# Optimization experiments

Measured on AMD Instinct MI355X. Metric: run time of the kernel, lower is better.

## Reference

```python
import jax, jax.numpy as jnp
import numpy as np

EPS_DIR = 1e-15
EPS_W = 1e-5
NEAR_MIN = 0.05


def setup_inputs() -> dict:
    key = jax.random.key(0)
    k1, k2, k3 = jax.random.split(key, 3)
    B, N, T = 1, 262144, 128
    rays_o = jax.random.normal(k1, (B, N, 3), dtype=jnp.float32)
    rays_d = jax.random.normal(k2, (B, N, 3), dtype=jnp.float32)
    weights = jax.random.uniform(k3, (B * N, T - 1), dtype=jnp.float32)
    return {"rays_o": rays_o, "rays_d": rays_d, "weights": weights,
            "bound": 1, "n_samples": 128}


def _near_far_cube(ro, rd, bound):
    # ro, rd: [R, 3]
    tmin = (-bound - ro) / (rd + EPS_DIR)
    tmax = (bound - ro) / (rd + EPS_DIR)
    near = jnp.max(jnp.minimum(tmin, tmax), axis=-1, keepdims=True)  # [R,1]
    far = jnp.min(jnp.maximum(tmin, tmax), axis=-1, keepdims=True)   # [R,1]
    near = jnp.maximum(near, NEAR_MIN)
    return near, far


def _sample_pdf(bins, weights, n_samples):
    # bins: [R, T], weights: [R, T-1]; deterministic (det=True) inverse-CDF sampling
    w = weights + EPS_W
    pdf = w / jnp.sum(w, axis=-1, keepdims=True)
    cdf = jnp.cumsum(pdf, axis=-1)
    cdf = jnp.concatenate([jnp.zeros_like(cdf[..., :1]), cdf], axis=-1)  # [R, T]
    n = n_samples
    u = jnp.linspace(0.5 / n, 1.0 - 0.5 / n, n, dtype=cdf.dtype)
    u = jnp.broadcast_to(u, cdf.shape[:-1] + (n,))                        # [R, n]
    inds = jax.vmap(lambda c, uu: jnp.searchsorted(c, uu, side='right'))(cdf, u)
    T = cdf.shape[-1]
    below = jnp.maximum(inds - 1, 0)
    above = jnp.minimum(inds, T - 1)
    cdf_lo = jnp.take_along_axis(cdf, below, axis=-1)
    cdf_hi = jnp.take_along_axis(cdf, above, axis=-1)
    bin_lo = jnp.take_along_axis(bins, below, axis=-1)
    bin_hi = jnp.take_along_axis(bins, above, axis=-1)
    denom = cdf_hi - cdf_lo
    denom = jnp.where(denom < EPS_W, jnp.ones_like(denom), denom)
    t = (u - cdf_lo) / denom
    return bin_lo + t * (bin_hi - bin_lo)  # [R, n]


def reference(rays_o, rays_d, weights, bound, n_samples):
    ro = rays_o.reshape(-1, 3)
    rd = rays_d.reshape(-1, 3)
    near, far = _near_far_cube(ro, rd, float(bound))          # [R,1]
    T = weights.shape[-1] + 1
    z = jnp.linspace(0.0, 1.0, T, dtype=ro.dtype)[None, :]    # [1,T]
    z_vals = near + (far - near) * z                          # [R,T] coarse bins
    new_z_vals = _sample_pdf(z_vals, weights, n_samples)      # [R,n_samples]
    return new_z_vals
```

## Files before the change

kernel.cpp:

```cpp
#include <hip/hip_runtime.h>

#define EPS_DIR 1e-15f
#define EPS_W   1e-5f
#define NEAR_MIN 0.05f

__global__ __launch_bounds__(256) void nerf_sample_pdf_kernel(
    const float* __restrict__ rays_o,
    const float* __restrict__ rays_d,
    const float* __restrict__ weights,
    const int*   __restrict__ bound_p,
    float*       __restrict__ out,
    int R, int Tm1, int n)
{
    const int lane = threadIdx.x & 63;
    const int wid  = threadIdx.x >> 6;
    int ray = blockIdx.x * 4 + wid;
    const bool valid = (ray < R);
    if (!valid) ray = R - 1;

    __shared__ float cdf_s[4][132];
    float* __restrict__ cdf = cdf_s[wid];

    const float* __restrict__ wrow = weights + (size_t)ray * Tm1;
    const int i0 = 2 * lane, i1 = 2 * lane + 1;
    float w0 = (i0 < Tm1) ? (wrow[i0] + EPS_W) : 0.0f;
    float w1 = (i1 < Tm1) ? (wrow[i1] + EPS_W) : 0.0f;

    float S = w0 + w1;
#pragma unroll
    for (int off = 1; off < 64; off <<= 1) {
        float y = __shfl_up(S, off, 64);
        if (lane >= off) S += y;
    }
    const float total = __shfl(S, 63, 64);
    const float rinv  = __builtin_amdgcn_rcpf(total);
    float prevS = __shfl_up(S, 1, 64);
    if (lane == 0) prevS = 0.0f;

    cdf[i0] = prevS * rinv;
    cdf[i1] = (prevS + w0) * rinv;
    __syncthreads();

    const float b = (float)bound_p[0];
    float nearv = -3.4e38f, farv = 3.4e38f;
#pragma unroll
    for (int k = 0; k < 3; ++k) {
        float o = rays_o[(size_t)ray * 3 + k];
        float d = rays_d[(size_t)ray * 3 + k] + EPS_DIR;
        float r = __builtin_amdgcn_rcpf(d);
        float t0 = (-b - o) * r;
        float t1 = ( b - o) * r;
        nearv = fmaxf(nearv, fminf(t0, t1));
        farv  = fminf(farv,  fmaxf(t0, t1));
    }
    nearv = fmaxf(nearv, NEAR_MIN);
    const float scale = (farv - nearv) * __builtin_amdgcn_rcpf((float)Tm1);
    const float inv_n = 1.0f / (float)n;

    float* __restrict__ orow = out + (size_t)ray * n;

    for (int base = 0; base < n; base += 128) {
        const int j = base + 2 * lane;
        if (j >= n) break;
        const float u0 = ((float)j + 0.5f) * inv_n;
        const float u1 = u0 + inv_n;

        int   p0 = 0,   p1 = 0;
        float v0 = 0.f, v1 = 0.f;
#pragma unroll
        for (int step = 64; step >= 1; step >>= 1) {
            const float c0 = cdf[p0 + step];
            const float c1 = cdf[p1 + step];
            if (c0 <= u0) { p0 += step; v0 = c0; }
            if (c1 <= u1) { p1 += step; v1 = c1; }
        }
        const int a0 = (p0 < Tm1) ? p0 + 1 : Tm1;
        const int a1 = (p1 < Tm1) ? p1 + 1 : Tm1;
        const float h0 = cdf[a0];
        const float h1 = cdf[a1];
        const float d0 = h0 - v0;
        const float d1 = h1 - v1;
        const float t0 = (u0 - v0) * ((d0 < EPS_W) ? 1.0f : __builtin_amdgcn_rcpf(d0));
        const float t1 = (u1 - v1) * ((d1 < EPS_W) ? 1.0f : __builtin_amdgcn_rcpf(d1));
        const float z0 = fmaf(t0, (float)(a0 - p0) * scale, fmaf((float)p0, scale, nearv));
        const float z1 = fmaf(t1, (float)(a1 - p1) * scale, fmaf((float)p1, scale, nearv));

        if (valid) {
            if (j + 1 < n) {
                *reinterpret_cast<float2*>(orow + j) = make_float2(z0, z1);
            } else {
                orow[j] = z0;
            }
        }
    }
}

extern "C" void kernel_launch(void* const* d_in, const int* in_sizes, int n_in,
                              void* d_out, int out_size, void* d_ws, size_t ws_size,
                              hipStream_t stream) {
    const float* rays_o  = (const float*)d_in[0];
    const float* rays_d  = (const float*)d_in[1];
    const float* weights = (const float*)d_in[2];
    const int*   bound_p = (const int*)d_in[3];
    float*       out     = (float*)d_out;

    const int R   = in_sizes[0] / 3;
    const int Tm1 = in_sizes[2] / R;
    const int n   = out_size / R;

    dim3 grid((R + 3) / 4), block(256);
    nerf_sample_pdf_kernel<<<grid, block, 0, stream>>>(
        rays_o, rays_d, weights, bound_p, out, R, Tm1, n);
}
```

Before: 295.4 us.

## Add specialized kernel mapping eight threads per ray for T=128 shapes

Adds a kernel for the 127-weight, 128-sample shape in which 8 threads share one ray. Each thread loads 16 weights, computes a serial local prefix and combines across the 8 threads with an xor shuffle scan, then does 16 binary searches and writes float4 stores. This replaces a full 64-lane shuffle scan per ray and gives 32 rays per block, at the cost of more registers per thread and strided, uncoalesced weight loads. The generic kernel also gains bounds guards on its search, and the host picks the path based on shape.

```diff
diff --git a/kernel.cpp b/kernel.cpp
--- a/kernel.cpp
+++ b/kernel.cpp
@@ -4,7 +4,103 @@
 #define EPS_W   1e-5f
 #define NEAR_MIN 0.05f
 
-__global__ __launch_bounds__(256) void nerf_sample_pdf_kernel(
+__global__ __launch_bounds__(256) void nerf_sample_pdf_127_128(
+    const float* __restrict__ rays_o,
+    const float* __restrict__ rays_d,
+    const float* __restrict__ weights,
+    const int*   __restrict__ bound_p,
+    float*       __restrict__ out,
+    int R)
+{
+    const int t    = threadIdx.x;
+    const int g    = t & 7;
+    const int rloc = t >> 3;
+    int ray = blockIdx.x * 32 + rloc;
+    const bool valid = (ray < R);
+    if (!valid) ray = R - 1;
+
+    __shared__ float cdf_s[32 * 132];
+    float* __restrict__ cdf = cdf_s + rloc * 132;
+
+    const float* __restrict__ wrow = weights + (size_t)ray * 127;
+    const int i0 = g << 4;
+    float w[16];
+#pragma unroll
+    for (int k = 0; k < 16; ++k) {
+        const int i = i0 + k;
+        w[k] = (i < 127) ? (wrow[i] + EPS_W) : 0.0f;
+    }
+
+    float local = w[0];
+#pragma unroll
+    for (int k = 1; k < 16; ++k) local += w[k];
+
+    float prefix = 0.0f, val = local;
+#pragma unroll
+    for (int k = 1; k < 8; k <<= 1) {
+        const float y = __shfl_xor(val, k, 8);
+        if (g & k) prefix += y;
+        val += y;
+    }
+    const float rtot = __builtin_amdgcn_rcpf(val);
+
+    if (g == 0) cdf[0] = 0.0f;
+    float run = prefix;
+#pragma unroll
+    for (int k = 0; k < 16; ++k) {
+        run += w[k];
+        cdf[i0 + k + 1] = run * rtot;
+    }
+
+    const float b = (float)bound_p[0];
+    float nearv = -3.4e38f, farv = 3.4e38f;
+#pragma unroll
+    for (int k = 0; k < 3; ++k) {
+        const float o = rays_o[(size_t)ray * 3 + k];
+        const float d = rays_d[(size_t)ray * 3 + k] + EPS_DIR;
+        const float r = __builtin_amdgcn_rcpf(d);
+        const float t0 = (-b - o) * r;
+        const float t1 = ( b - o) * r;
+        nearv = fmaxf(nearv, fminf(t0, t1));
+        farv  = fminf(farv,  fmaxf(t0, t1));
+    }
+    nearv = fmaxf(nearv, NEAR_MIN);
+    const float scale = (farv - nearv) * (1.0f / 127.0f);
+
+    float* __restrict__ orow = out + (size_t)ray * 128;
+    const float inv_n = 1.0f / 128.0f;
+
+#pragma unroll
+    for (int q = 0; q < 4; ++q) {
+        float z0, z1, z2, z3;
+#pragma unroll
+        for (int s = 0; s < 4; ++s) {
+            const int j = i0 + 4 * q + s;
+            const float u = ((float)j + 0.5f) * inv_n;
+            int p = 0; float v = 0.0f;
+#pragma unroll
+            for (int step = 64; step >= 1; step >>= 1) {
+                const float c = cdf[p + step];
+                if (c <= u) { p += step; v = c; }
+            }
+            const float h   = cdf[p + 1];
+            const float dnm = h - v;
+            const float rd  = (dnm < EPS_W) ? 1.0f : __builtin_amdgcn_rcpf(dnm);
+            const float tt  = (u - v) * rd;
+            const float z   = fmaf((float)p + tt, scale, nearv);
+            if      (s == 0) z0 = z;
+            else if (s == 1) z1 = z;
+            else if (s == 2) z2 = z;
+            else             z3 = z;
+        }
+        if (valid) {
+            *reinterpret_cast<float4*>(orow + i0 + 4 * q) =
+                make_float4(z0, z1, z2, z3);
+        }
+    }
+}
+
+__global__ __launch_bounds__(256) void nerf_sample_pdf_generic(
     const float* __restrict__ rays_o,
     const float* __restrict__ rays_d,
     const float* __restrict__ weights,
@@ -69,10 +165,14 @@
         float v0 = 0.f, v1 = 0.f;
 #pragma unroll
         for (int step = 64; step >= 1; step >>= 1) {
-            const float c0 = cdf[p0 + step];
-            const float c1 = cdf[p1 + step];
-            if (c0 <= u0) { p0 += step; v0 = c0; }
-            if (c1 <= u1) { p1 += step; v1 = c1; }
+            if (p0 + step <= Tm1) {
+                const float c0 = cdf[p0 + step];
+                if (c0 <= u0) { p0 += step; v0 = c0; }
+            }
+            if (p1 + step <= Tm1) {
+                const float c1 = cdf[p1 + step];
+                if (c1 <= u1) { p1 += step; v1 = c1; }
+            }
         }
         const int a0 = (p0 < Tm1) ? p0 + 1 : Tm1;
         const int a1 = (p1 < Tm1) ? p1 + 1 : Tm1;
@@ -108,7 +208,13 @@
     const int Tm1 = in_sizes[2] / R;
     const int n   = out_size / R;
 
-    dim3 grid((R + 3) / 4), block(256);
-    nerf_sample_pdf_kernel<<<grid, block, 0, stream>>>(
-        rays_o, rays_d, weights, bound_p, out, R, Tm1, n);
+    if (Tm1 == 127 && n == 128) {
+        dim3 grid((R + 31) / 32), block(256);
+        nerf_sample_pdf_127_128<<<grid, block, 0, stream>>>(
+            rays_o, rays_d, weights, bound_p, out, R);
+    } else {
+        dim3 grid((R + 3) / 4), block(256);
+        nerf_sample_pdf_generic<<<grid, block, 0, stream>>>(
+            rays_o, rays_d, weights, bound_p, out, R, Tm1, n);
+    }
 }
```

After: 258.1 us. 12.6% less time.
